# Kernel optimization log

Measured on AMD Instinct MI355X. Metric: run time of the kernel, lower is better.

Reference implementation:

```python
import jax, jax.numpy as jnp
import numpy as np

N_NODES = 500_000
N_ELEM = 2_000_000
W_AXIAL = 1.0
W_BENDING = 1.0


def _local_axes(x_local):
    # ref = [0,1,0] unless nearly parallel to x, then [0,0,1]
    parallel = jnp.abs(x_local[:, 1]) > 0.99
    ref = jnp.where(parallel[:, None],
                    jnp.array([0.0, 0.0, 1.0], x_local.dtype),
                    jnp.array([0.0, 1.0, 0.0], x_local.dtype))
    z = jnp.cross(x_local, ref)
    z = z / jnp.maximum(jnp.linalg.norm(z, axis=-1, keepdims=True), 1e-8)
    y = jnp.cross(z, x_local)
    y = y / jnp.maximum(jnp.linalg.norm(y, axis=-1, keepdims=True), 1e-8)
    return y, z


def setup_inputs() -> dict:
    key = jax.random.key(0)
    ks = jax.random.split(key, 10)
    pred = jax.random.normal(ks[0], (N_NODES, 6), jnp.float32) * 0.01
    connectivity = jax.random.randint(ks[1], (N_ELEM, 2), 0, N_NODES, dtype=jnp.int32)
    d = jax.random.normal(ks[2], (N_ELEM, 3), jnp.float32)
    elem_directions = d / jnp.linalg.norm(d, axis=-1, keepdims=True)
    elem_lengths = jax.random.uniform(ks[3], (N_ELEM,), jnp.float32, 0.5, 5.0)
    prop_E = jax.random.uniform(ks[4], (N_ELEM,), jnp.float32, 1e5, 2e6)
    prop_A = jax.random.uniform(ks[5], (N_ELEM,), jnp.float32, 0.01, 0.1)
    prop_I22 = jax.random.uniform(ks[6], (N_ELEM,), jnp.float32, 1e-5, 1e-3)
    line_load = jax.random.normal(ks[7], (N_NODES, 3), jnp.float32)
    bc_disp = jax.random.uniform(ks[8], (N_NODES, 1), jnp.float32)
    bc_rot = jax.random.uniform(ks[9], (N_NODES, 1), jnp.float32)
    return dict(pred=pred, connectivity=connectivity, elem_directions=elem_directions,
                elem_lengths=elem_lengths, prop_E=prop_E, prop_A=prop_A,
                prop_I22=prop_I22, line_load=line_load, bc_disp=bc_disp, bc_rot=bc_rot)


def reference(pred, connectivity, elem_directions, elem_lengths,
              prop_E, prop_A, prop_I22, line_load, bc_disp, bc_rot):
    n_nodes = pred.shape[0]
    u = pred[:, :3]
    theta = pred[:, 3:6]
    i_nodes = connectivity[:, 0]
    j_nodes = connectivity[:, 1]
    x_local = elem_directions
    y_local, z_local = _local_axes(x_local)
    L = elem_lengths

    du = u[j_nodes] - u[i_nodes]            # (E,3)
    th_i = theta[i_nodes]
    th_j = theta[j_nodes]

    # axial
    axial_disp = jnp.sum(du * x_local, axis=-1)
    N_axial = prop_E * prop_A / L * axial_disp
    F_axial_vec = N_axial[:, None] * x_local

    EI = prop_E * prop_I22
    L2 = L * L
    L3 = L2 * L

    # bending: transverse z (rotations about y)
    dw_z = jnp.sum(du * z_local, axis=-1)
    theta_yi = jnp.sum(th_i * y_local, axis=-1)
    theta_yj = jnp.sum(th_j * y_local, axis=-1)
    V_z = 12.0 * EI / L3 * dw_z + 6.0 * EI / L2 * (theta_yi + theta_yj)
    F_shear_vec = V_z[:, None] * z_local
    M_yi = 6.0 * EI / L2 * dw_z + EI / L * (2.0 * theta_yi + theta_yj)
    M_yj = 6.0 * EI / L2 * dw_z + EI / L * (theta_yi + 2.0 * theta_yj)
    M_vec_i = M_yi[:, None] * y_local
    M_vec_j = M_yj[:, None] * y_local

    # bending: transverse y (rotations about z)
    dw_y = jnp.sum(du * y_local, axis=-1)
    theta_zi = jnp.sum(th_i * z_local, axis=-1)
    theta_zj = jnp.sum(th_j * z_local, axis=-1)
    V_y = 12.0 * EI / L3 * dw_y + 6.0 * EI / L2 * (theta_zi + theta_zj)
    F_shear_y_vec = V_y[:, None] * y_local
    M_zi = 6.0 * EI / L2 * dw_y + EI / L * (2.0 * theta_zi + theta_zj)
    M_zj = 6.0 * EI / L2 * dw_y + EI / L * (theta_zi + 2.0 * theta_zj)
    M_vec_zi = M_zi[:, None] * z_local
    M_vec_zj = M_zj[:, None] * z_local

    # scatter to nodes (combined contributions, same sum as six scatter_adds)
    F_contrib = F_axial_vec + F_shear_vec + F_shear_y_vec
    F_total = jnp.zeros((n_nodes, 3), pred.dtype)
    F_total = F_total.at[i_nodes].add(F_contrib).at[j_nodes].add(-F_contrib)
    F_residual = F_total + line_load

    M_total = jnp.zeros((n_nodes, 3), pred.dtype)
    M_total = M_total.at[i_nodes].add(M_vec_i + M_vec_zi).at[j_nodes].add(M_vec_j + M_vec_zj)

    # characteristic scales
    F_char = jnp.maximum(jnp.mean(prop_E * prop_A), 1.0)
    M_char = jnp.maximum(jnp.mean(prop_E * prop_I22 / L), 1.0)

    # masked means over free nodes (== boolean-indexed .mean() in torch)
    free_disp = (bc_disp[:, 0] < 0.5).astype(pred.dtype)   # (N,)
    free_rot = (bc_rot[:, 0] < 0.5).astype(pred.dtype)
    sq_f = (F_residual / F_char) ** 2
    sq_m = (M_total / M_char) ** 2
    loss_force = jnp.sum(sq_f * free_disp[:, None]) / jnp.maximum(jnp.sum(free_disp) * 3.0, 1.0)
    loss_moment = jnp.sum(sq_m * free_rot[:, None]) / jnp.maximum(jnp.sum(free_rot) * 3.0, 1.0)
    return W_AXIAL * loss_force + W_BENDING * loss_moment
```

## Files before the change

### kernel.cpp

```cpp
#include <hip/hip_runtime.h>
#include <hip/hip_bf16.h>

#define N_NODES 500000
#define N_ELEM  2000000

#define CSH   11
#define NPBIN (1 << CSH)
#define NBIN  ((N_NODES + NPBIN - 1) >> CSH)
#define SBLK  256
#define CBLK  512

#define ENT_OFF 32768ull
#define WS_NEED (ENT_OFF + 16ull * 2 * N_ELEM)

__device__ __forceinline__ float wave_reduce(float v) {
    #pragma unroll
    for (int o = 32; o > 0; o >>= 1) v += __shfl_down(v, o, 64);
    return v;
}

template<int NW>
__device__ __forceinline__ void block_reduce_add(float v, double* dst, float* sm) {
    int lane = threadIdx.x & 63;
    int wave = threadIdx.x >> 6;
    v = wave_reduce(v);
    if (lane == 0) sm[wave] = v;
    __syncthreads();
    if (threadIdx.x == 0) {
        float s = 0.f;
        #pragma unroll
        for (int w = 0; w < NW; ++w) s += sm[w];
        atomicAdd(dst, (double)s);
    }
    __syncthreads();
}

__device__ __forceinline__ unsigned int pack2(float a, float b) {
    unsigned int ua = (__float_as_uint(a) + 0x8000u) >> 16;
    unsigned int ub = (__float_as_uint(b) + 0x8000u) & 0xFFFF0000u;
    return ua | ub;
}
__device__ __forceinline__ float unlo(unsigned int u) {
    return __uint_as_float(u << 16);
}
__device__ __forceinline__ float unhi(unsigned int u) {
    return __uint_as_float(u & 0xFFFF0000u);
}

__device__ __forceinline__ void beam_full(
    float x0, float x1, float x2,
    const float* __restrict__ pi, const float* __restrict__ pj,
    float L, float E, float A, float I,
    float& F0, float& F1, float& F2,
    float& Mi0, float& Mi1, float& Mi2,
    float& Mj0, float& Mj1, float& Mj2)
{
    bool par = fabsf(x1) > 0.99f;
    float r1 = par ? 0.f : 1.f;
    float r2 = par ? 1.f : 0.f;
    float z0 = x1 * r2 - x2 * r1;
    float z1 = -x0 * r2;
    float z2 = x0 * r1;
    float zn = fmaxf(sqrtf(z0 * z0 + z1 * z1 + z2 * z2), 1e-8f);
    float izn = 1.f / zn;
    z0 *= izn; z1 *= izn; z2 *= izn;
    float y0 = z1 * x2 - z2 * x1;
    float y1 = z2 * x0 - z0 * x2;
    float y2 = z0 * x1 - z1 * x0;
    float yn = fmaxf(sqrtf(y0 * y0 + y1 * y1 + y2 * y2), 1e-8f);
    float iyn = 1.f / yn;
    y0 *= iyn; y1 *= iyn; y2 *= iyn;

    float2 a0 = *(const float2*)(pi + 0);
    float2 a1 = *(const float2*)(pi + 2);
    float2 a2 = *(const float2*)(pi + 4);
    float2 b0 = *(const float2*)(pj + 0);
    float2 b1 = *(const float2*)(pj + 2);
    float2 b2 = *(const float2*)(pj + 4);
    float du0 = b0.x - a0.x;
    float du1 = b0.y - a0.y;
    float du2 = b1.x - a1.x;
    float ti0 = a1.y, ti1 = a2.x, ti2 = a2.y;
    float tj0 = b1.y, tj1 = b2.x, tj2 = b2.y;

    float EA = E * A;
    float EI = E * I;
    float invL = 1.f / L;
    float invL2 = invL * invL;
    float invL3 = invL2 * invL;

    float axial = du0 * x0 + du1 * x1 + du2 * x2;
    float Naxial = EA * invL * axial;

    float k12 = 12.f * EI * invL3;
    float k6  = 6.f * EI * invL2;
    float kL  = EI * invL;

    float dwz = du0 * z0 + du1 * z1 + du2 * z2;
    float tyi = ti0 * y0 + ti1 * y1 + ti2 * y2;
    float tyj = tj0 * y0 + tj1 * y1 + tj2 * y2;
    float Vz  = k12 * dwz + k6 * (tyi + tyj);
    float Myi = k6 * dwz + kL * (2.f * tyi + tyj);
    float Myj = k6 * dwz + kL * (tyi + 2.f * tyj);

    float dwy = du0 * y0 + du1 * y1 + du2 * y2;
    float tzi = ti0 * z0 + ti1 * z1 + ti2 * z2;
    float tzj = tj0 * z0 + tj1 * z1 + tj2 * z2;
    float Vy  = k12 * dwy + k6 * (tzi + tzj);
    float Mzi = k6 * dwy + kL * (2.f * tzi + tzj);
    float Mzj = k6 * dwy + kL * (tzi + 2.f * tzj);

    F0 = Naxial * x0 + Vz * z0 + Vy * y0;
    F1 = Naxial * x1 + Vz * z1 + Vy * y1;
    F2 = Naxial * x2 + Vz * z2 + Vy * y2;

    Mi0 = Myi * y0 + Mzi * z0;
    Mi1 = Myi * y1 + Mzi * z1;
    Mi2 = Myi * y2 + Mzi * z2;
    Mj0 = Myj * y0 + Mzj * z0;
    Mj1 = Myj * y1 + Mzj * z1;
    Mj2 = Myj * y2 + Mzj * z2;
}


__global__ __launch_bounds__(256) void count_kernel(
    const int* __restrict__ conn, int* __restrict__ cnt)
{
    __shared__ int bins[NBIN];
    for (int i = threadIdx.x; i < NBIN; i += 256) bins[i] = 0;
    __syncthreads();

    int per = (N_ELEM + CBLK - 1) / CBLK;
    int e0 = blockIdx.x * per;
    int e1 = min(e0 + per, N_ELEM);
    const int2* c2 = (const int2*)conn;

    for (int e = e0 + threadIdx.x; e < e1; e += 256) {
        int2 c = c2[e];
        atomicAdd(&bins[c.x >> CSH], 1);
        atomicAdd(&bins[c.y >> CSH], 1);
    }
    __syncthreads();
    for (int i = threadIdx.x; i < NBIN; i += 256) {
        int c = bins[i];
        if (c) atomicAdd(&cnt[i], c);
    }
}

__global__ __launch_bounds__(256) void scan_kernel(
    const int* __restrict__ cnt,
    int* __restrict__ cur, int* __restrict__ off)
{
    __shared__ int s[256];
    int tid = threadIdx.x;
    int v = (tid < NBIN) ? cnt[tid] : 0;
    s[tid] = v;
    __syncthreads();
    for (int o = 1; o < 256; o <<= 1) {
        int t = (tid >= o) ? s[tid - o] : 0;
        __syncthreads();
        s[tid] += t;
        __syncthreads();
    }
    int excl = s[tid] - v;
    if (tid < NBIN) { off[tid] = excl; cur[tid] = excl; }
    if (tid == 255) off[NBIN] = s[255];
}


__global__ __launch_bounds__(1024) void emit_kernel(
    const float* __restrict__ pred,
    const int* __restrict__ conn,
    const float* __restrict__ dirs,
    const float* __restrict__ L_, const float* __restrict__ E_,
    const float* __restrict__ A_, const float* __restrict__ I_,
    int* __restrict__ cur, uint4* __restrict__ ents,
    double* __restrict__ accum)
{
    __shared__ int bins[NBIN];
    __shared__ float sm[16];
    for (int i = threadIdx.x; i < NBIN; i += 1024) bins[i] = 0;
    __syncthreads();

    int per = (N_ELEM + SBLK - 1) / SBLK;
    int e0 = blockIdx.x * per;
    int e1 = min(e0 + per, N_ELEM);
    const int2* c2 = (const int2*)conn;

    for (int e = e0 + threadIdx.x; e < e1; e += 1024) {
        int2 c = c2[e];
        atomicAdd(&bins[c.x >> CSH], 1);
        atomicAdd(&bins[c.y >> CSH], 1);
    }
    __syncthreads();
    for (int i = threadIdx.x; i < NBIN; i += 1024) {
        int c = bins[i];
        bins[i] = c ? atomicAdd(&cur[i], c) : 0;
    }
    __syncthreads();

    float ea = 0.f, eil = 0.f;
    for (int e = e0 + threadIdx.x; e < e1; e += 1024) {
        int2 c = c2[e];
        float x0 = dirs[3 * e + 0], x1 = dirs[3 * e + 1], x2 = dirs[3 * e + 2];
        float L = L_[e], E = E_[e], A = A_[e], I = I_[e];
        ea  += E * A;
        eil += E * I / L;
        float F0, F1, F2, Mi0, Mi1, Mi2, Mj0, Mj1, Mj2;
        beam_full(x0, x1, x2, pred + 6l * c.x, pred + 6l * c.y, L, E, A, I,
                  F0, F1, F2, Mi0, Mi1, Mi2, Mj0, Mj1, Mj2);

        int pi_ = atomicAdd(&bins[c.x >> CSH], 1);
        uint4 ei;
        ei.x = pack2(F0, F1);
        ei.y = pack2(F2, Mi0);
        ei.z = pack2(Mi1, Mi2);
        ei.w = (unsigned int)(c.x & (NPBIN - 1));
        ents[pi_] = ei;

        int pj_ = atomicAdd(&bins[c.y >> CSH], 1);
        uint4 ej;
        ej.x = pack2(-F0, -F1);
        ej.y = pack2(-F2, Mj0);
        ej.z = pack2(Mj1, Mj2);
        ej.w = (unsigned int)(c.y & (NPBIN - 1));
        ents[pj_] = ej;
    }
    block_reduce_add<16>(ea,  &accum[0], sm);
    block_reduce_add<16>(eil, &accum[1], sm);
}


__global__ __launch_bounds__(1024) void binacc_kernel(
    const uint4* __restrict__ ents,
    const int* __restrict__ off,
    const float* __restrict__ line_load,
    const float* __restrict__ bc_disp,
    const float* __restrict__ bc_rot,
    double* __restrict__ accum)
{
    __shared__ unsigned int acc3[NPBIN * 3];
    __shared__ float sm[16];
    int b = blockIdx.x;
    for (int i = threadIdx.x; i < NPBIN * 3; i += 1024) acc3[i] = 0u;
    __syncthreads();

    int s0 = off[b], s1 = off[b + 1];
    int nbase = b << CSH;
    unsigned int lds_base = (unsigned int)(unsigned long long)(&acc3[0]);

    int k = s0 + threadIdx.x;
    for (; k + 1024 < s1; k += 2048) {
        uint4 ea_ = ents[k];
        uint4 eb_ = ents[k + 1024];
        unsigned int aa = lds_base + ea_.w * 12u;
        unsigned int ab = lds_base + eb_.w * 12u;
        asm volatile(
            "ds_pk_add_bf16 %0, %2\n\t"
            "ds_pk_add_bf16 %0, %3 offset:4\n\t"
            "ds_pk_add_bf16 %0, %4 offset:8\n\t"
            "ds_pk_add_bf16 %1, %5\n\t"
            "ds_pk_add_bf16 %1, %6 offset:4\n\t"
            "ds_pk_add_bf16 %1, %7 offset:8"
            :: "v"(aa), "v"(ab),
               "v"(ea_.x), "v"(ea_.y), "v"(ea_.z),
               "v"(eb_.x), "v"(eb_.y), "v"(eb_.z)
            : "memory");
    }
    if (k < s1) {
        uint4 e = ents[k];
        unsigned int a = lds_base + e.w * 12u;
        asm volatile(
            "ds_pk_add_bf16 %0, %1\n\t"
            "ds_pk_add_bf16 %0, %2 offset:4\n\t"
            "ds_pk_add_bf16 %0, %3 offset:8"
            :: "v"(a), "v"(e.x), "v"(e.y), "v"(e.z)
            : "memory");
    }
    asm volatile("s_waitcnt lgkmcnt(0)" ::: "memory");
    __syncthreads();

    float sqF = 0.f, sqM = 0.f, fd = 0.f, fr = 0.f;
    for (int nl = threadIdx.x; nl < NPBIN; nl += 1024) {
        int n = nbase + nl;
        if (n < N_NODES) {
            float fdv = (bc_disp[n] < 0.5f) ? 1.f : 0.f;
            float frv = (bc_rot[n]  < 0.5f) ? 1.f : 0.f;
            unsigned int w0 = acc3[nl * 3 + 0];
            unsigned int w1 = acc3[nl * 3 + 1];
            unsigned int w2 = acc3[nl * 3 + 2];
            float Fr0 = unlo(w0) + line_load[3l * n + 0];
            float Fr1 = unhi(w0) + line_load[3l * n + 1];
            float Fr2 = unlo(w1) + line_load[3l * n + 2];
            float M0 = unhi(w1);
            float M1 = unlo(w2);
            float M2 = unhi(w2);
            sqF += fdv * (Fr0 * Fr0 + Fr1 * Fr1 + Fr2 * Fr2);
            sqM += frv * (M0 * M0 + M1 * M1 + M2 * M2);
            fd += fdv;
            fr += frv;
        }
    }
    block_reduce_add<16>(sqF, &accum[2], sm);
    block_reduce_add<16>(sqM, &accum[3], sm);
    block_reduce_add<16>(fd,  &accum[4], sm);
    block_reduce_add<16>(fr,  &accum[5], sm);
}

__global__ void final_kernel(const double* __restrict__ accum,
                             float* __restrict__ out)
{
    double F_char = fmax(accum[0] / (double)N_ELEM, 1.0);
    double M_char = fmax(accum[1] / (double)N_ELEM, 1.0);
    double lf = accum[2] / (F_char * F_char) / fmax(accum[4] * 3.0, 1.0);
    double lm = accum[3] / (M_char * M_char) / fmax(accum[5] * 3.0, 1.0);
    out[0] = (float)(lf + lm);
}


__global__ __launch_bounds__(256) void elem_kernel_fb(
    const float* __restrict__ pred,
    const int*   __restrict__ conn,
    const float* __restrict__ dirs,
    const float* __restrict__ L_, const float* __restrict__ E_,
    const float* __restrict__ A_, const float* __restrict__ I_,
    float* __restrict__ F_total, float* __restrict__ M_total,
    double* __restrict__ accum)
{
    __shared__ float sm[4];
    int e = blockIdx.x * blockDim.x + threadIdx.x;
    float ea = 0.f, eil = 0.f;
    if (e < N_ELEM) {
        int ni = conn[2 * e], nj = conn[2 * e + 1];
        float x0 = dirs[3 * e + 0], x1 = dirs[3 * e + 1], x2 = dirs[3 * e + 2];
        float L = L_[e], E = E_[e], A = A_[e], I = I_[e];
        float F0, F1, F2, Mi0, Mi1, Mi2, Mj0, Mj1, Mj2;
        beam_full(x0, x1, x2, pred + 6l * ni, pred + 6l * nj, L, E, A, I,
                  F0, F1, F2, Mi0, Mi1, Mi2, Mj0, Mj1, Mj2);
        atomicAdd(&F_total[3l * ni + 0],  F0);
        atomicAdd(&F_total[3l * ni + 1],  F1);
        atomicAdd(&F_total[3l * ni + 2],  F2);
        atomicAdd(&F_total[3l * nj + 0], -F0);
        atomicAdd(&F_total[3l * nj + 1], -F1);
        atomicAdd(&F_total[3l * nj + 2], -F2);
        atomicAdd(&M_total[3l * ni + 0], Mi0);
        atomicAdd(&M_total[3l * ni + 1], Mi1);
        atomicAdd(&M_total[3l * ni + 2], Mi2);
        atomicAdd(&M_total[3l * nj + 0], Mj0);
        atomicAdd(&M_total[3l * nj + 1], Mj1);
        atomicAdd(&M_total[3l * nj + 2], Mj2);
        ea  = E * A;
        eil = E * I / L;
    }
    block_reduce_add<4>(ea,  &accum[0], sm);
    block_reduce_add<4>(eil, &accum[1], sm);
}

__global__ __launch_bounds__(256) void node_kernel_fb(
    const float* __restrict__ F_total, const float* __restrict__ M_total,
    const float* __restrict__ line_load,
    const float* __restrict__ bc_disp, const float* __restrict__ bc_rot,
    double* __restrict__ accum)
{
    __shared__ float sm[4];
    int n = blockIdx.x * blockDim.x + threadIdx.x;
    float sqF = 0.f, sqM = 0.f, fd = 0.f, fr = 0.f;
    if (n < N_NODES) {
        fd = (bc_disp[n] < 0.5f) ? 1.f : 0.f;
        fr = (bc_rot[n]  < 0.5f) ? 1.f : 0.f;
        float Fr0 = F_total[3l * n + 0] + line_load[3l * n + 0];
        float Fr1 = F_total[3l * n + 1] + line_load[3l * n + 1];
        float Fr2 = F_total[3l * n + 2] + line_load[3l * n + 2];
        float M0 = M_total[3l * n + 0];
        float M1 = M_total[3l * n + 1];
        float M2 = M_total[3l * n + 2];
        sqF = fd * (Fr0 * Fr0 + Fr1 * Fr1 + Fr2 * Fr2);
        sqM = fr * (M0 * M0 + M1 * M1 + M2 * M2);
    }
    block_reduce_add<4>(sqF, &accum[2], sm);
    block_reduce_add<4>(sqM, &accum[3], sm);
    block_reduce_add<4>(fd,  &accum[4], sm);
    block_reduce_add<4>(fr,  &accum[5], sm);
}

extern "C" void kernel_launch(void* const* d_in, const int* in_sizes, int n_in,
                              void* d_out, int out_size, void* d_ws, size_t ws_size,
                              hipStream_t stream) {
    const float* pred      = (const float*)d_in[0];
    const int*   conn      = (const int*)  d_in[1];
    const float* dirs      = (const float*)d_in[2];
    const float* lens      = (const float*)d_in[3];
    const float* prop_E    = (const float*)d_in[4];
    const float* prop_A    = (const float*)d_in[5];
    const float* prop_I    = (const float*)d_in[6];
    const float* line_load = (const float*)d_in[7];
    const float* bc_disp   = (const float*)d_in[8];
    const float* bc_rot    = (const float*)d_in[9];

    double* accum = (double*)d_ws;

    if (ws_size >= WS_NEED) {
        int* off = (int*)((char*)d_ws + 1024);
        int* cnt = (int*)((char*)d_ws + 8192);
        int* cur = (int*)((char*)d_ws + 16384);
        uint4* ents = (uint4*)((char*)d_ws + ENT_OFF);

        hipMemsetAsync(d_ws, 0, 32768, stream);

        count_kernel<<<CBLK, 256, 0, stream>>>(conn, cnt);
        scan_kernel<<<1, 256, 0, stream>>>(cnt, cur, off);
        emit_kernel<<<SBLK, 1024, 0, stream>>>(pred, conn, dirs, lens,
                                               prop_E, prop_A, prop_I,
                                               cur, ents, accum);
        binacc_kernel<<<NBIN, 1024, 0, stream>>>(ents, off, line_load, bc_disp,
                                                 bc_rot, accum);
    } else {
        float* F_total = (float*)((char*)d_ws + 64);
        float* M_total = F_total + (size_t)N_NODES * 3;
        hipMemsetAsync(d_ws, 0, 64 + 2ull * N_NODES * 3 * sizeof(float), stream);
        int be = (N_ELEM + 255) / 256;
        elem_kernel_fb<<<be, 256, 0, stream>>>(pred, conn, dirs, lens, prop_E,
                                               prop_A, prop_I, F_total, M_total, accum);
        int bn = (N_NODES + 255) / 256;
        node_kernel_fb<<<bn, 256, 0, stream>>>(F_total, M_total, line_load,
                                               bc_disp, bc_rot, accum);
    }
    final_kernel<<<1, 1, 0, stream>>>(accum, (float*)d_out);
}
```

Measured before the change: 214.2 us.

## Vectorize emit kernel loads and batch node gathers four elements per thread

Emit kernel now processes four consecutive elements per thread using float4/int4 loads for connectivity, directions and properties, and issues all pred gathers before the compute for more memory-level parallelism. Grid changes from 256×1024 to many 512-thread blocks of 4096 elements each. This adds register pressure and a scalar tail path.

```diff
diff --git a/kernel.cpp b/kernel.cpp
--- a/kernel.cpp
+++ b/kernel.cpp
@@ -7,7 +7,8 @@
 #define CSH   11
 #define NPBIN (1 << CSH)
 #define NBIN  ((N_NODES + NPBIN - 1) >> CSH)
-#define SBLK  256
+#define EPB   4096
+#define EBLK  ((N_ELEM + EPB - 1) / EPB)
 #define CBLK  512
 
 #define ENT_OFF 32768ull
@@ -47,9 +48,10 @@
     return __uint_as_float(u & 0xFFFF0000u);
 }
 
-__device__ __forceinline__ void beam_full(
+__device__ __forceinline__ void beam_core(
     float x0, float x1, float x2,
-    const float* __restrict__ pi, const float* __restrict__ pj,
+    float2 a0, float2 a1, float2 a2,
+    float2 b0, float2 b1, float2 b2,
     float L, float E, float A, float I,
     float& F0, float& F1, float& F2,
     float& Mi0, float& Mi1, float& Mi2,
@@ -71,55 +73,67 @@
     float iyn = 1.f / yn;
     y0 *= iyn; y1 *= iyn; y2 *= iyn;
 
+    float du0 = b0.x - a0.x;
+    float du1 = b0.y - a0.y;
+    float du2 = b1.x - a1.x;
+    float ti0 = a1.y, ti1 = a2.x, ti2 = a2.y;
+    float tj0 = b1.y, tj1 = b2.x, tj2 = b2.y;
+
+    float EA = E * A;
+    float EI = E * I;
+    float invL = 1.f / L;
+    float invL2 = invL * invL;
+    float invL3 = invL2 * invL;
+
+    float axial = du0 * x0 + du1 * x1 + du2 * x2;
+    float Naxial = EA * invL * axial;
+
+    float k12 = 12.f * EI * invL3;
+    float k6  = 6.f * EI * invL2;
+    float kL  = EI * invL;
+
+    float dwz = du0 * z0 + du1 * z1 + du2 * z2;
+    float tyi = ti0 * y0 + ti1 * y1 + ti2 * y2;
+    float tyj = tj0 * y0 + tj1 * y1 + tj2 * y2;
+    float Vz  = k12 * dwz + k6 * (tyi + tyj);
+    float Myi = k6 * dwz + kL * (2.f * tyi + tyj);
+    float Myj = k6 * dwz + kL * (tyi + 2.f * tyj);
+
+    float dwy = du0 * y0 + du1 * y1 + du2 * y2;
+    float tzi = ti0 * z0 + ti1 * z1 + ti2 * z2;
+    float tzj = tj0 * z0 + tj1 * z1 + tj2 * z2;
+    float Vy  = k12 * dwy + k6 * (tzi + tzj);
+    float Mzi = k6 * dwy + kL * (2.f * tzi + tzj);
+    float Mzj = k6 * dwy + kL * (tzi + 2.f * tzj);
+
+    F0 = Naxial * x0 + Vz * z0 + Vy * y0;
+    F1 = Naxial * x1 + Vz * z1 + Vy * y1;
+    F2 = Naxial * x2 + Vz * z2 + Vy * y2;
+
+    Mi0 = Myi * y0 + Mzi * z0;
+    Mi1 = Myi * y1 + Mzi * z1;
+    Mi2 = Myi * y2 + Mzi * z2;
+    Mj0 = Myj * y0 + Mzj * z0;
+    Mj1 = Myj * y1 + Mzj * z1;
+    Mj2 = Myj * y2 + Mzj * z2;
+}
+
+__device__ __forceinline__ void beam_full(
+    float x0, float x1, float x2,
+    const float* __restrict__ pi, const float* __restrict__ pj,
+    float L, float E, float A, float I,
+    float& F0, float& F1, float& F2,
+    float& Mi0, float& Mi1, float& Mi2,
+    float& Mj0, float& Mj1, float& Mj2)
+{
     float2 a0 = *(const float2*)(pi + 0);
     float2 a1 = *(const float2*)(pi + 2);
     float2 a2 = *(const float2*)(pi + 4);
     float2 b0 = *(const float2*)(pj + 0);
     float2 b1 = *(const float2*)(pj + 2);
     float2 b2 = *(const float2*)(pj + 4);
-    float du0 = b0.x - a0.x;
-    float du1 = b0.y - a0.y;
-    float du2 = b1.x - a1.x;
-    float ti0 = a1.y, ti1 = a2.x, ti2 = a2.y;
-    float tj0 = b1.y, tj1 = b2.x, tj2 = b2.y;
-
-    float EA = E * A;
-    float EI = E * I;
-    float invL = 1.f / L;
-    float invL2 = invL * invL;
-    float invL3 = invL2 * invL;
-
-    float axial = du0 * x0 + du1 * x1 + du2 * x2;
-    float Naxial = EA * invL * axial;
-
-    float k12 = 12.f * EI * invL3;
-    float k6  = 6.f * EI * invL2;
-    float kL  = EI * invL;
-
-    float dwz = du0 * z0 + du1 * z1 + du2 * z2;
-    float tyi = ti0 * y0 + ti1 * y1 + ti2 * y2;
-    float tyj = tj0 * y0 + tj1 * y1 + tj2 * y2;
-    float Vz  = k12 * dwz + k6 * (tyi + tyj);
-    float Myi = k6 * dwz + kL * (2.f * tyi + tyj);
-    float Myj = k6 * dwz + kL * (tyi + 2.f * tyj);
-
-    float dwy = du0 * y0 + du1 * y1 + du2 * y2;
-    float tzi = ti0 * z0 + ti1 * z1 + ti2 * z2;
-    float tzj = tj0 * z0 + tj1 * z1 + tj2 * z2;
-    float Vy  = k12 * dwy + k6 * (tzi + tzj);
-    float Mzi = k6 * dwy + kL * (2.f * tzi + tzj);
-    float Mzj = k6 * dwy + kL * (tzi + 2.f * tzj);
-
-    F0 = Naxial * x0 + Vz * z0 + Vy * y0;
-    F1 = Naxial * x1 + Vz * z1 + Vy * y1;
-    F2 = Naxial * x2 + Vz * z2 + Vy * y2;
-
-    Mi0 = Myi * y0 + Mzi * z0;
-    Mi1 = Myi * y1 + Mzi * z1;
-    Mi2 = Myi * y2 + Mzi * z2;
-    Mj0 = Myj * y0 + Mzj * z0;
-    Mj1 = Myj * y1 + Mzj * z1;
-    Mj2 = Myj * y2 + Mzj * z2;
+    beam_core(x0, x1, x2, a0, a1, a2, b0, b1, b2, L, E, A, I,
+              F0, F1, F2, Mi0, Mi1, Mi2, Mj0, Mj1, Mj2);
 }
 
 
@@ -168,7 +182,7 @@
 }
 
 
-__global__ __launch_bounds__(1024) void emit_kernel(
+__global__ __launch_bounds__(512) void emit_kernel(
     const float* __restrict__ pred,
     const int* __restrict__ conn,
     const float* __restrict__ dirs,
@@ -178,38 +192,100 @@
     double* __restrict__ accum)
 {
     __shared__ int bins[NBIN];
-    __shared__ float sm[16];
-    for (int i = threadIdx.x; i < NBIN; i += 1024) bins[i] = 0;
-    __syncthreads();
-
-    int per = (N_ELEM + SBLK - 1) / SBLK;
-    int e0 = blockIdx.x * per;
-    int e1 = min(e0 + per, N_ELEM);
+    __shared__ float sm[8];
+    for (int i = threadIdx.x; i < NBIN; i += 512) bins[i] = 0;
+    __syncthreads();
+
+    int e0 = blockIdx.x * EPB;
+    int e1 = min(e0 + EPB, N_ELEM);
     const int2* c2 = (const int2*)conn;
-
-    for (int e = e0 + threadIdx.x; e < e1; e += 1024) {
+    const int4* c4 = (const int4*)conn;
+
+    for (int e = e0 + threadIdx.x; e < e1; e += 512) {
         int2 c = c2[e];
         atomicAdd(&bins[c.x >> CSH], 1);
         atomicAdd(&bins[c.y >> CSH], 1);
     }
     __syncthreads();
-    for (int i = threadIdx.x; i < NBIN; i += 1024) {
+    for (int i = threadIdx.x; i < NBIN; i += 512) {
         int c = bins[i];
         bins[i] = c ? atomicAdd(&cur[i], c) : 0;
     }
     __syncthreads();
 
     float ea = 0.f, eil = 0.f;
-    for (int e = e0 + threadIdx.x; e < e1; e += 1024) {
-        int2 c = c2[e];
-        float x0 = dirs[3 * e + 0], x1 = dirs[3 * e + 1], x2 = dirs[3 * e + 2];
-        float L = L_[e], E = E_[e], A = A_[e], I = I_[e];
+
+    int e = e0 + threadIdx.x * 4;
+    #pragma unroll 1
+    for (int m = 0; m < 2; ++m, e += 2048) {
+        if (e + 3 >= e1) break;
+        int4 ca = c4[e >> 1];
+        int4 cb = c4[(e >> 1) + 1];
+        int cx[4] = {ca.x, ca.z, cb.x, cb.z};
+        int cy[4] = {ca.y, ca.w, cb.y, cb.w};
+
+        const float4* d4 = (const float4*)(dirs + 3 * e);
+        float4 d0 = d4[0], d1 = d4[1], d2 = d4[2];
+        float fl[12] = {d0.x, d0.y, d0.z, d0.w, d1.x, d1.y,
+                        d1.z, d1.w, d2.x, d2.y, d2.z, d2.w};
+
+        float4 Lv = *(const float4*)(L_ + e);
+        float4 Ev = *(const float4*)(E_ + e);
+        float4 Av = *(const float4*)(A_ + e);
+        float4 Iv = *(const float4*)(I_ + e);
+        float Ls[4] = {Lv.x, Lv.y, Lv.z, Lv.w};
+        float Es[4] = {Ev.x, Ev.y, Ev.z, Ev.w};
+        float As[4] = {Av.x, Av.y, Av.z, Av.w};
+        float Is[4] = {Iv.x, Iv.y, Iv.z, Iv.w};
+
+        float2 pa0[4], pa1[4], pa2[4], pb0[4], pb1[4], pb2[4];
+        #pragma unroll
+        for (int u = 0; u < 4; ++u) {
+            const float2* pi2 = (const float2*)(pred + 6l * cx[u]);
+            const float2* pj2 = (const float2*)(pred + 6l * cy[u]);
+            pa0[u] = pi2[0]; pa1[u] = pi2[1]; pa2[u] = pi2[2];
+            pb0[u] = pj2[0]; pb1[u] = pj2[1]; pb2[u] = pj2[2];
+        }
+
+        #pragma unroll
+        for (int u = 0; u < 4; ++u) {
+            float L = Ls[u], E = Es[u], A = As[u], I = Is[u];
+            ea  += E * A;
+            eil += E * I / L;
+            float F0, F1, F2, Mi0, Mi1, Mi2, Mj0, Mj1, Mj2;
+            beam_core(fl[3 * u], fl[3 * u + 1], fl[3 * u + 2],
+                      pa0[u], pa1[u], pa2[u], pb0[u], pb1[u], pb2[u],
+                      L, E, A, I,
+                      F0, F1, F2, Mi0, Mi1, Mi2, Mj0, Mj1, Mj2);
+
+            int pi_ = atomicAdd(&bins[cx[u] >> CSH], 1);
+            uint4 ei;
+            ei.x = pack2(F0, F1);
+            ei.y = pack2(F2, Mi0);
+            ei.z = pack2(Mi1, Mi2);
+            ei.w = (unsigned int)(cx[u] & (NPBIN - 1));
+            ents[pi_] = ei;
+
+            int pj_ = atomicAdd(&bins[cy[u] >> CSH], 1);
+            uint4 ej;
+            ej.x = pack2(-F0, -F1);
+            ej.y = pack2(-F2, Mj0);
+            ej.z = pack2(Mj1, Mj2);
+            ej.w = (unsigned int)(cy[u] & (NPBIN - 1));
+            ents[pj_] = ej;
+        }
+    }
+
+    int qend = e0 + ((e1 - e0) & ~3);
+    for (int es = qend + threadIdx.x; es < e1; es += 512) {
+        int2 c = c2[es];
+        float x0 = dirs[3 * es + 0], x1 = dirs[3 * es + 1], x2 = dirs[3 * es + 2];
+        float L = L_[es], E = E_[es], A = A_[es], I = I_[es];
         ea  += E * A;
         eil += E * I / L;
         float F0, F1, F2, Mi0, Mi1, Mi2, Mj0, Mj1, Mj2;
         beam_full(x0, x1, x2, pred + 6l * c.x, pred + 6l * c.y, L, E, A, I,
                   F0, F1, F2, Mi0, Mi1, Mi2, Mj0, Mj1, Mj2);
-
         int pi_ = atomicAdd(&bins[c.x >> CSH], 1);
         uint4 ei;
         ei.x = pack2(F0, F1);
@@ -217,7 +293,6 @@
         ei.z = pack2(Mi1, Mi2);
         ei.w = (unsigned int)(c.x & (NPBIN - 1));
         ents[pi_] = ei;
-
         int pj_ = atomicAdd(&bins[c.y >> CSH], 1);
         uint4 ej;
         ej.x = pack2(-F0, -F1);
@@ -226,8 +301,9 @@
         ej.w = (unsigned int)(c.y & (NPBIN - 1));
         ents[pj_] = ej;
     }
-    block_reduce_add<16>(ea,  &accum[0], sm);
-    block_reduce_add<16>(eil, &accum[1], sm);
+
+    block_reduce_add<8>(ea,  &accum[0], sm);
+    block_reduce_add<8>(eil, &accum[1], sm);
 }
 
 
@@ -409,9 +485,9 @@
 
         count_kernel<<<CBLK, 256, 0, stream>>>(conn, cnt);
         scan_kernel<<<1, 256, 0, stream>>>(cnt, cur, off);
-        emit_kernel<<<SBLK, 1024, 0, stream>>>(pred, conn, dirs, lens,
-                                               prop_E, prop_A, prop_I,
-                                               cur, ents, accum);
+        emit_kernel<<<EBLK, 512, 0, stream>>>(pred, conn, dirs, lens,
+                                              prop_E, prop_A, prop_I,
+                                              cur, ents, accum);
         binacc_kernel<<<NBIN, 1024, 0, stream>>>(ents, off, line_load, bc_disp,
                                                  bc_rot, accum);
     } else {
```

New measurement: 216.3 us. Within noise of the previous version (+0.9%).
